# Performance work log

Measured on AMD Instinct MI355X. Metric: run time of the kernel, lower is better.

The kernel has to match this reference:

```python
import jax, jax.numpy as jnp
import numpy as np

V, D, H, O = 500000, 64, 64, 64
N0, N1, N2, K = 8192, 100000, 300000, 32


def setup_inputs() -> dict:
    key = jax.random.key(0)
    ks = jax.random.split(key, 8)
    return {
        "feats": jax.random.normal(ks[0], (V, D), dtype=jnp.float32),
        "W0": jax.random.normal(ks[1], (D, H), dtype=jnp.float32) / jnp.sqrt(jnp.float32(D)),
        "b0": jnp.zeros((H,), jnp.float32),
        "W1": jax.random.normal(ks[2], (H, O), dtype=jnp.float32) / jnp.sqrt(jnp.float32(H)),
        "b1": jnp.zeros((O,), jnp.float32),
        "neigh_idx0": jax.random.randint(ks[3], (N0, K), 0, N1),  # seed -> positions in 1-hop layer
        "neigh_idx1": jax.random.randint(ks[4], (N1, K), 0, N2),  # 1-hop -> positions in 2-hop layer
        "node_ids1": jax.random.randint(ks[5], (N1,), 0, V),      # 1-hop node ids into feature table
        "node_ids2": jax.random.randint(ks[6], (N2,), 0, V),      # 2-hop node ids into feature table
    }


def reference(feats, W0, b0, W1, b1, neigh_idx0, neigh_idx1, node_ids1, node_ids2):
    # Embedding lookups (self.features(...)) for hop-1 and hop-2 node layers.
    v1 = feats[node_ids1]                       # [N1, D]
    v2 = feats[node_ids2]                       # [N2, D]
    # Layer i=0, hop=1: mean over sampled neighbors (mask.mm == gather-mean),
    # then linear0 + relu (dropout in eval mode == identity).
    agg1 = jnp.mean(v2[neigh_idx1], axis=1)     # [N1, D]
    h1 = jax.nn.relu(agg1 @ W0 + b0)            # [N1, H]
    # Layer i=1, hop=0: aggregate hop-1 representations for seed nodes, linear1 + relu.
    agg0 = jnp.mean(h1[neigh_idx0], axis=1)     # [N0, H]
    out = jax.nn.relu(agg0 @ W1 + b1)           # [N0, O]
    return out
```

## Files before the change

### kernel.cpp

```cpp
#include <hip/hip_runtime.h>
#include <hip/hip_bf16.h>

typedef __hip_bfloat16 bf16;

static __device__ __forceinline__ float lane_bcast_f(float v, int l) {
    return __uint_as_float(__builtin_amdgcn_readlane(__float_as_uint(v), l));
}

template <typename HT>
__global__ __launch_bounds__(256) void k_hop1(
    const float* __restrict__ feats,
    const float* __restrict__ W0,
    const float* __restrict__ b0,
    const int*   __restrict__ idx1,
    const int*   __restrict__ nid2,
    HT*          __restrict__ h1,
    int N1)
{
    const int lane  = threadIdx.x & 63;
    const int gwave = blockIdx.x * (blockDim.x >> 6) + (threadIdx.x >> 6);
    const int nwave = gridDim.x * (blockDim.x >> 6);

    float w0[64];
#pragma unroll
    for (int d = 0; d < 64; ++d) w0[d] = W0[d * 64 + lane];
    const float bias = b0[lane];

    for (int row = gwave; row < N1; row += nwave) {
        const int j   = idx1[row * 32 + (lane & 31)];
        const int nid = nid2[j];

        float acc = 0.f;
#pragma unroll
        for (int k = 0; k < 32; ++k) {
            const int nk = __builtin_amdgcn_readlane(nid, k);
            acc += feats[(size_t)nk * 64 + lane];
        }
        const float agg = acc * 0.03125f;

        float h = bias;
#pragma unroll
        for (int d = 0; d < 64; ++d)
            h = fmaf(lane_bcast_f(agg, d), w0[d], h);
        h = fmaxf(h, 0.f);
        if constexpr (sizeof(HT) == 2)
            h1[(size_t)row * 64 + lane] = __float2bfloat16(h);
        else
            h1[(size_t)row * 64 + lane] = h;
    }
}

template <typename HT>
__global__ __launch_bounds__(256) void k_hop0(
    const HT*    __restrict__ h1,
    const float* __restrict__ W1,
    const float* __restrict__ b1,
    const int*   __restrict__ idx0,
    float*       __restrict__ out,
    int N0)
{
    const int lane  = threadIdx.x & 63;
    const int gwave = blockIdx.x * (blockDim.x >> 6) + (threadIdx.x >> 6);
    const int nwave = gridDim.x * (blockDim.x >> 6);

    float w1[64];
#pragma unroll
    for (int d = 0; d < 64; ++d) w1[d] = W1[d * 64 + lane];
    const float bias = b1[lane];

    for (int row = gwave; row < N0; row += nwave) {
        const int j = idx0[row * 32 + (lane & 31)];

        float acc = 0.f;
#pragma unroll
        for (int k = 0; k < 32; ++k) {
            const int jk = __builtin_amdgcn_readlane(j, k);
            float v;
            if constexpr (sizeof(HT) == 2)
                v = __bfloat162float(h1[(size_t)jk * 64 + lane]);
            else
                v = h1[(size_t)jk * 64 + lane];
            acc += v;
        }
        const float agg = acc * 0.03125f;

        float o = bias;
#pragma unroll
        for (int d = 0; d < 64; ++d)
            o = fmaf(lane_bcast_f(agg, d), w1[d], o);
        o = fmaxf(o, 0.f);
        out[(size_t)row * 64 + lane] = o;
    }
}

extern "C" void kernel_launch(void* const* d_in, const int* in_sizes, int n_in,
                              void* d_out, int out_size, void* d_ws, size_t ws_size,
                              hipStream_t stream) {
    const float* feats = (const float*)d_in[0];
    const float* W0    = (const float*)d_in[1];
    const float* b0    = (const float*)d_in[2];
    const float* W1    = (const float*)d_in[3];
    const float* b1    = (const float*)d_in[4];
    const int*   idx0  = (const int*)d_in[5];
    const int*   idx1  = (const int*)d_in[6];
    const int*   nid2  = (const int*)d_in[8];

    const int N0 = in_sizes[5] / 32;
    const int N1 = in_sizes[6] / 32;

    const size_t need_f32 = (size_t)N1 * 64 * sizeof(float);

    if (ws_size >= need_f32) {
        float* h1 = (float*)d_ws;
        k_hop1<float><<<2048, 256, 0, stream>>>(feats, W0, b0, idx1, nid2, h1, N1);
        k_hop0<float><<<512, 256, 0, stream>>>(h1, W1, b1, idx0, (float*)d_out, N0);
    } else {
        bf16* h1 = (bf16*)d_ws;
        k_hop1<bf16><<<2048, 256, 0, stream>>>(feats, W0, b0, idx1, nid2, h1, N1);
        k_hop0<bf16><<<512, 256, 0, stream>>>(h1, W1, b1, idx0, (float*)d_out, N0);
    }
}
```

Measured before the change: 313.9 us.

## Vectorize neighbor gathers to float4 and process two rows per wave

Restructures both hop kernels so each wave loads neighbor feature rows as float4 (16 lanes per row, 4 neighbors in parallel) instead of one scalar per lane, then reduces the partial sums across lane groups with xor shuffles. The hop-1 kernel handles two output rows per wave, which doubles the memory requests in flight to hide gather latency. The hop-0 grid is enlarged. This adds shuffle reduction work and register pressure in exchange for wider, more concurrent loads.

```diff
diff --git a/kernel.cpp b/kernel.cpp
--- a/kernel.cpp
+++ b/kernel.cpp
@@ -5,6 +5,19 @@
 
 static __device__ __forceinline__ float lane_bcast_f(float v, int l) {
     return __uint_as_float(__builtin_amdgcn_readlane(__float_as_uint(v), l));
+}
+
+static __device__ __forceinline__ float4 load4f(const float* p) {
+    return *(const float4*)p;
+}
+static __device__ __forceinline__ float4 load4f(const bf16* p) {
+    const ushort4 s = *(const ushort4*)p;
+    float4 r;
+    r.x = __uint_as_float((unsigned)s.x << 16);
+    r.y = __uint_as_float((unsigned)s.y << 16);
+    r.z = __uint_as_float((unsigned)s.z << 16);
+    r.w = __uint_as_float((unsigned)s.w << 16);
+    return r;
 }
 
 template <typename HT>
@@ -17,36 +30,72 @@
     HT*          __restrict__ h1,
     int N1)
 {
-    const int lane  = threadIdx.x & 63;
+    const int lane = threadIdx.x & 63;
+    const int sub  = lane >> 4;
+    const int c4   = lane & 15;
     const int gwave = blockIdx.x * (blockDim.x >> 6) + (threadIdx.x >> 6);
     const int nwave = gridDim.x * (blockDim.x >> 6);
 
-    float w0[64];
+    float w0c[64];
 #pragma unroll
-    for (int d = 0; d < 64; ++d) w0[d] = W0[d * 64 + lane];
+    for (int d = 0; d < 64; ++d) w0c[d] = W0[d * 64 + lane];
     const float bias = b0[lane];
 
-    for (int row = gwave; row < N1; row += nwave) {
-        const int j   = idx1[row * 32 + (lane & 31)];
-        const int nid = nid2[j];
+    const float4* f4 = (const float4*)feats;
 
-        float acc = 0.f;
+    for (int base = 2 * gwave; base < N1; base += 2 * nwave) {
+        const int r0 = base;
+        const bool has_r1 = (base + 1 < N1);
+        const int r1 = has_r1 ? base + 1 : base;
+
+        int nk0[8], nk1[8];
 #pragma unroll
-        for (int k = 0; k < 32; ++k) {
-            const int nk = __builtin_amdgcn_readlane(nid, k);
-            acc += feats[(size_t)nk * 64 + lane];
+        for (int i = 0; i < 8; ++i) {
+            nk0[i] = idx1[r0 * 32 + 4 * i + sub];
+            nk1[i] = idx1[r1 * 32 + 4 * i + sub];
         }
-        const float agg = acc * 0.03125f;
+#pragma unroll
+        for (int i = 0; i < 8; ++i) {
+            nk0[i] = nid2[nk0[i]];
+            nk1[i] = nid2[nk1[i]];
+        }
 
-        float h = bias;
+        float a0[4] = {0.f, 0.f, 0.f, 0.f};
+        float a1[4] = {0.f, 0.f, 0.f, 0.f};
 #pragma unroll
-        for (int d = 0; d < 64; ++d)
-            h = fmaf(lane_bcast_f(agg, d), w0[d], h);
-        h = fmaxf(h, 0.f);
-        if constexpr (sizeof(HT) == 2)
-            h1[(size_t)row * 64 + lane] = __float2bfloat16(h);
-        else
-            h1[(size_t)row * 64 + lane] = h;
+        for (int i = 0; i < 8; ++i) {
+            const float4 v0 = f4[(size_t)nk0[i] * 16 + c4];
+            const float4 v1 = f4[(size_t)nk1[i] * 16 + c4];
+            a0[0] += v0.x; a0[1] += v0.y; a0[2] += v0.z; a0[3] += v0.w;
+            a1[0] += v1.x; a1[1] += v1.y; a1[2] += v1.z; a1[3] += v1.w;
+        }
+
+#pragma unroll
+        for (int c = 0; c < 4; ++c) {
+            a0[c] += __shfl_xor(a0[c], 16, 64);
+            a0[c] += __shfl_xor(a0[c], 32, 64);
+            a1[c] += __shfl_xor(a1[c], 16, 64);
+            a1[c] += __shfl_xor(a1[c], 32, 64);
+            a0[c] *= 0.03125f;
+            a1[c] *= 0.03125f;
+        }
+
+        float h0 = bias, h1v = bias;
+#pragma unroll
+        for (int d = 0; d < 64; ++d) {
+            h0  = fmaf(lane_bcast_f(a0[d & 3], d >> 2), w0c[d], h0);
+            h1v = fmaf(lane_bcast_f(a1[d & 3], d >> 2), w0c[d], h1v);
+        }
+        h0  = fmaxf(h0, 0.f);
+        h1v = fmaxf(h1v, 0.f);
+
+        if constexpr (sizeof(HT) == 2) {
+            h1[(size_t)r0 * 64 + lane] = __float2bfloat16(h0);
+            if (has_r1) h1[(size_t)r1 * 64 + lane] = __float2bfloat16(h1v);
+        } else {
+            h1[(size_t)r0 * 64 + lane] = h0;
+            if (has_r1) h1[(size_t)r1 * 64 + lane] = h1v;
+        }
     }
 }
 
@@ -59,37 +108,40 @@
     float*       __restrict__ out,
     int N0)
 {
-    const int lane  = threadIdx.x & 63;
+    const int lane = threadIdx.x & 63;
+    const int sub  = lane >> 4;
+    const int c4   = lane & 15;
     const int gwave = blockIdx.x * (blockDim.x >> 6) + (threadIdx.x >> 6);
     const int nwave = gridDim.x * (blockDim.x >> 6);
 
-    float w1[64];
+    float w1c[64];
 #pragma unroll
-    for (int d = 0; d < 64; ++d) w1[d] = W1[d * 64 + lane];
+    for (int d = 0; d < 64; ++d) w1c[d] = W1[d * 64 + lane];
     const float bias = b1[lane];
 
     for (int row = gwave; row < N0; row += nwave) {
-        const int j = idx0[row * 32 + (lane & 31)];
+        int jk[8];
+#pragma unroll
+        for (int i = 0; i < 8; ++i) jk[i] = idx0[row * 32 + 4 * i + sub];
 
-        float acc = 0.f;
+        float a[4] = {0.f, 0.f, 0.f, 0.f};
 #pragma unroll
-        for (int k = 0; k < 32; ++k) {
-            const int jk = __builtin_amdgcn_readlane(j, k);
-            float v;
-            if constexpr (sizeof(HT) == 2)
-                v = __bfloat162float(h1[(size_t)jk * 64 + lane]);
-            else
-                v = h1[(size_t)jk * 64 + lane];
-            acc += v;
+        for (int i = 0; i < 8; ++i) {
+            const float4 v = load4f(h1 + (size_t)jk[i] * 64 + c4 * 4);
+            a[0] += v.x; a[1] += v.y; a[2] += v.z; a[3] += v.w;
         }
-        const float agg = acc * 0.03125f;
+#pragma unroll
+        for (int c = 0; c < 4; ++c) {
+            a[c] += __shfl_xor(a[c], 16, 64);
+            a[c] += __shfl_xor(a[c], 32, 64);
+            a[c] *= 0.03125f;
+        }
 
         float o = bias;
 #pragma unroll
         for (int d = 0; d < 64; ++d)
-            o = fmaf(lane_bcast_f(agg, d), w1[d], o);
-        o = fmaxf(o, 0.f);
-        out[(size_t)row * 64 + lane] = o;
+            o = fmaf(lane_bcast_f(a[d & 3], d >> 2), w1c[d], o);
+        out[(size_t)row * 64 + lane] = fmaxf(o, 0.f);
     }
 }
 
@@ -113,10 +165,10 @@
     if (ws_size >= need_f32) {
         float* h1 = (float*)d_ws;
         k_hop1<float><<<2048, 256, 0, stream>>>(feats, W0, b0, idx1, nid2, h1, N1);
-        k_hop0<float><<<512, 256, 0, stream>>>(h1, W1, b1, idx0, (float*)d_out, N0);
+        k_hop0<float><<<2048, 256, 0, stream>>>(h1, W1, b1, idx0, (float*)d_out, N0);
     } else {
         bf16* h1 = (bf16*)d_ws;
         k_hop1<bf16><<<2048, 256, 0, stream>>>(feats, W0, b0, idx1, nid2, h1, N1);
-        k_hop0<bf16><<<512, 256, 0, stream>>>(h1, W1, b1, idx0, (float*)d_out, N0);
+        k_hop0<bf16><<<2048, 256, 0, stream>>>(h1, W1, b1, idx0, (float*)d_out, N0);
     }
 }
```

New measurement: 316.6 us. No clear change (+0.9%).
